# Performance work log

Hardware: AMD Instinct MI355X
Metric: run time of the kernel (lower is better)

The kernel has to match this reference:

```python
import jax, jax.numpy as jnp
import numpy as np

N_NODES = 100000
N_GRAPHS = 256
N_EDGES = 800000


def gcn_conv(x, W, b, src, dst):
    """PyG GCNConv: self-loops + symmetric deg^-1/2 normalization + scatter-add."""
    h = x @ W  # [N, F_out]
    # degree on graph with self-loops (edge weight 1)
    deg = jax.ops.segment_sum(jnp.ones((src.shape[0],), h.dtype), dst,
                              num_segments=N_NODES) + 1.0
    dinv = jax.lax.rsqrt(deg)  # deg^-1/2, deg >= 1 so finite
    norm = dinv[src] * dinv[dst]  # [E]
    msg = h[src] * norm[:, None]  # gather + scale, [E, F_out]
    agg = jax.ops.segment_sum(msg, dst, num_segments=N_NODES)
    # self-loop contribution: dinv[i]^2 * h[i]
    agg = agg + h * (dinv * dinv)[:, None]
    return agg + b


def setup_inputs() -> dict:
    key = jax.random.key(0)
    ks = jax.random.split(key, 16)
    inp = {
        "x": jax.random.normal(ks[0], (N_NODES, 114), jnp.float32),
        "edge_index": jax.random.randint(ks[1], (2, N_EDGES), 0, N_NODES, jnp.int64)
        if jax.config.jax_enable_x64 else jax.random.randint(ks[1], (2, N_EDGES), 0, N_NODES, jnp.int32),
        "batch": jnp.sort(jax.random.randint(ks[2], (N_NODES,), 0, N_GRAPHS,
                                             jnp.int32)),
        "W1": jax.random.normal(ks[3], (114, 230), jnp.float32) * 0.09,
        "b1": jax.random.normal(ks[4], (230,), jnp.float32) * 0.01,
        "W2": jax.random.normal(ks[5], (230, 115), jnp.float32) * 0.07,
        "b2": jax.random.normal(ks[6], (115,), jnp.float32) * 0.01,
        "Wg": jax.random.normal(ks[7], (115, 64), jnp.float32) * 0.09,
        "bg": jax.random.normal(ks[8], (64,), jnp.float32) * 0.01,
        "Wf": jax.random.normal(ks[9], (64, 32), jnp.float32) * 0.12,
        "bf": jax.random.normal(ks[10], (32,), jnp.float32) * 0.01,
        "Wo": jax.random.normal(ks[11], (32, 1), jnp.float32) * 0.17,
        "bo": jax.random.normal(ks[12], (1,), jnp.float32) * 0.01,
    }
    return inp


def reference(x, edge_index, batch, W1, b1, W2, b2, Wg, bg, Wf, bf, Wo, bo):
    src, dst = edge_index[0], edge_index[1]
    h = jax.nn.relu(gcn_conv(x, W1, b1, src, dst))
    # dropout p=0.2 is identity at inference (training=False)
    h = jax.nn.relu(gcn_conv(h, W2, b2, src, dst))
    # global max pool over graphs; h >= 0 after relu so clamp empty segments to 0
    pooled = jax.ops.segment_max(h, batch, num_segments=N_GRAPHS)
    pooled = jnp.maximum(pooled, 0.0)  # [G, 115]
    g = jax.nn.relu(pooled @ Wg + bg)
    g = jax.nn.relu(g @ Wf + bf)
    return g @ Wo + bo  # [G, 1]
```

## Files before the change

kernel.cpp:

```cpp
#include <hip/hip_runtime.h>
#include <hip/hip_bf16.h>
#include <hip/hip_fp16.h>

#define NN 100000
#define NG 256
#define NE 800000

constexpr int F0 = 114;
constexpr int F1 = 230;
constexpr int F2 = 115;
constexpr int MPAD = 100096;

typedef _Float16 __attribute__((ext_vector_type(8))) f16x8;
typedef __attribute__((ext_vector_type(4))) float f32x4;
typedef __attribute__((ext_vector_type(8))) unsigned short u16x8;

__device__ __forceinline__ unsigned short f2h_bits(float x) {
  _Float16 h = (_Float16)x;
  return __builtin_bit_cast(unsigned short, h);
}
__device__ __forceinline__ float h_bits2f(unsigned short u) {
  return (float)__builtin_bit_cast(_Float16, u);
}


__global__ void k_count(const int* __restrict__ dst, int* __restrict__ cnt) {
  int e = blockIdx.x * blockDim.x + threadIdx.x;
  if (e < NE) atomicAdd(&cnt[dst[e]], 1);
}

__global__ void k_dinv(const int* __restrict__ cnt, float* __restrict__ dinv) {
  int i = blockIdx.x * blockDim.x + threadIdx.x;
  if (i < NN) dinv[i] = rsqrtf((float)cnt[i] + 1.0f);
}

constexpr int SCAN_T = 256;
constexpr int SCAN_E = 1024;
constexpr int NB = (NN + SCAN_E - 1) / SCAN_E;

__global__ void k_scan1(const int* __restrict__ cnt, int* __restrict__ off,
                        int* __restrict__ bsum) {
  __shared__ int s[SCAN_T];
  int b = blockIdx.x, t = threadIdx.x;
  int base = b * SCAN_E + t * 4;
  int v0 = 0, v1 = 0, v2 = 0, v3 = 0;
  if (base + 0 < NN) v0 = cnt[base + 0];
  if (base + 1 < NN) v1 = cnt[base + 1];
  if (base + 2 < NN) v2 = cnt[base + 2];
  if (base + 3 < NN) v3 = cnt[base + 3];
  int sum = v0 + v1 + v2 + v3;
  s[t] = sum;
  __syncthreads();
  for (int ofs = 1; ofs < SCAN_T; ofs <<= 1) {
    int x = (t >= ofs) ? s[t - ofs] : 0;
    __syncthreads();
    s[t] += x;
    __syncthreads();
  }
  int excl = s[t] - sum;
  if (base + 0 < NN) off[base + 0] = excl;
  if (base + 1 < NN) off[base + 1] = excl + v0;
  if (base + 2 < NN) off[base + 2] = excl + v0 + v1;
  if (base + 3 < NN) off[base + 3] = excl + v0 + v1 + v2;
  if (t == SCAN_T - 1) bsum[b] = s[t];
}

__global__ void k_scan2(int* bsum) {
  __shared__ int ws[2];
  int t = threadIdx.x;
  int v = (t < NB) ? bsum[t] : 0;
  int orig = v;
  for (int o = 1; o < 64; o <<= 1) {
    int x = __shfl_up(v, o, 64);
    if ((t & 63) >= o) v += x;
  }
  if ((t & 63) == 63) ws[t >> 6] = v;
  __syncthreads();
  if (t >= 64) v += ws[0];
  if (t < NB) bsum[t] = v - orig;
}

__global__ void k_scan3(int* __restrict__ off, const int* __restrict__ bsum,
                        int* __restrict__ cur) {
  int i = blockIdx.x * blockDim.x + threadIdx.x;
  if (i < NN) {
    int v = off[i] + bsum[i / SCAN_E];
    off[i] = v;
    cur[i] = v;
  }
  if (i == NN) off[NN] = NE;
}

__global__ void k_place(const int* __restrict__ src, const int* __restrict__ dst,
                        int* __restrict__ cur, int* __restrict__ srcs) {
  int e = blockIdx.x * blockDim.x + threadIdx.x;
  if (e >= NE) return;
  int p = atomicAdd(&cur[dst[e]], 1);
  srcs[p] = src[e];
}


__global__ void k_prepx(const float* __restrict__ x, const float* __restrict__ dinv,
                        unsigned short* __restrict__ xd) {
  int n = blockIdx.x, f = threadIdx.x;
  float v = (f < F0) ? x[(size_t)n * F0 + f] * dinv[n] : 0.0f;
  xd[(size_t)n * 128 + f] = f2h_bits(v);
}


template <bool POOL>
__global__ __launch_bounds__(256) void k_gatherw(
    const unsigned short* __restrict__ tab, const float* __restrict__ dinv,
    const int* __restrict__ off, const int* __restrict__ srcs,
    const float* __restrict__ b2, const int* __restrict__ batch,
    unsigned short* __restrict__ outh, float* __restrict__ pooled) {
  __shared__ float smax[4][128];
  __shared__ int sg[4];
  int w = threadIdx.x >> 6, lane = threadIdx.x & 63;
  int n = blockIdx.x * 4 + w;
  int grp = lane >> 4, sub = lane & 15;
  int fb = sub * 8;

  float acc[8] = {0.f, 0.f, 0.f, 0.f, 0.f, 0.f, 0.f, 0.f};
  int j0 = off[n], j1 = off[n + 1];
  for (int base = j0; base <= j1; base += 16) {
    int row[4];
    u16x8 v[4];
    bool has[4];
#pragma unroll
    for (int c = 0; c < 4; ++c) {
      int je = base + c * 4 + grp;
      row[c] = (je < j1) ? srcs[je] : ((je == j1) ? n : -1);
      has[c] = row[c] >= 0;
    }
#pragma unroll
    for (int c = 0; c < 4; ++c)
      if (has[c]) v[c] = *(const u16x8*)&tab[(size_t)row[c] * 128 + fb];
#pragma unroll
    for (int c = 0; c < 4; ++c)
      if (has[c]) {
#pragma unroll
        for (int u = 0; u < 8; ++u) acc[u] += h_bits2f(v[c][u]);
      }
  }
#pragma unroll
  for (int u = 0; u < 8; ++u) {
    acc[u] += __shfl_xor(acc[u], 16);
    acc[u] += __shfl_xor(acc[u], 32);
  }
  float dn = dinv[n];

  if constexpr (!POOL) {
    if (grp == 0) {
      u16x8 o;
#pragma unroll
      for (int u = 0; u < 8; ++u) o[u] = f2h_bits(acc[u] * dn);
      *(u16x8*)&outh[(size_t)n * 128 + fb] = o;
    }
  } else {
    if (grp == 0) {
#pragma unroll
      for (int u = 0; u < 8; ++u) {
        int f = fb + u;
        float bb = (f < F2) ? b2[f] : 0.0f;
        smax[w][f] = fmaxf(acc[u] * dn + bb, 0.0f);
      }
      if (sub == 0) sg[w] = batch[n];
    }
    __syncthreads();
    int t = threadIdx.x;
    if (t < 128) {
      int g0 = sg[0];
      bool same = (sg[1] == g0) & (sg[2] == g0) & (sg[3] == g0);
      if (same) {
        float m = fmaxf(fmaxf(smax[0][t], smax[1][t]),
                        fmaxf(smax[2][t], smax[3][t]));
        if (t < F2 && m > 0.0f)
          atomicMax((int*)&pooled[g0 * F2 + t], __float_as_int(m));
      } else {
        for (int ww = 0; ww < 4; ++ww) {
          float m = smax[ww][t];
          if (t < F2 && m > 0.0f)
            atomicMax((int*)&pooled[sg[ww] * F2 + t], __float_as_int(m));
        }
      }
    }
  }
}


__global__ void k_prepB(const float* __restrict__ W, unsigned short* __restrict__ Bh,
                        unsigned short* __restrict__ Bl, int K, int N, int KP) {
  int n = blockIdx.x, k = threadIdx.x;
  float v = (k < K && n < N) ? W[(size_t)k * N + n] : 0.0f;
  unsigned short h = f2h_bits(v);
  unsigned short l = f2h_bits(v - h_bits2f(h));
  Bh[(size_t)n * KP + k] = h;
  Bl[(size_t)n * KP + k] = l;
}


__global__ __launch_bounds__(256, 3) void k_fused(
    const unsigned short* __restrict__ A,
    const unsigned short* __restrict__ B1h, const unsigned short* __restrict__ B1l,
    const unsigned short* __restrict__ B2h, const unsigned short* __restrict__ B2l,
    const float* __restrict__ b1, const float* __restrict__ dscale,
    unsigned short* __restrict__ td) {
  __shared__ char lds[49152];
  char* h1B = lds;
  char* Bs0 = lds + 16384;
  char* Bs1 = lds + 32768;

  const int t = threadIdx.x;
  const int m0 = blockIdx.x * 64;
  const int lane = t & 63, w = t >> 6;
  const int r = lane & 15;
  const int kq = lane >> 4;
  const int kb2 = kq * 16;
  const int kbu = kq * 8;
  const int rq = kq * 4;
  const int wc = w * 32;
  const int brow = t >> 1, bseg = t & 1;
  const int rb = brow * 128, swb = (brow & 7) << 4;

  const unsigned short* Ath = A + (size_t)(m0 + r) * 128 + kbu;

  f32x4 acc2[4][2];
#pragma unroll
  for (int i = 0; i < 4; ++i)
#pragma unroll
    for (int j = 0; j < 2; ++j) acc2[i][j] = (f32x4){0.f, 0.f, 0.f, 0.f};

  for (int h = 0; h < 2; ++h) {
    f32x4 acc[4][2];
#pragma unroll
    for (int i = 0; i < 4; ++i)
#pragma unroll
      for (int j = 0; j < 2; ++j) acc[i][j] = (f32x4){0.f, 0.f, 0.f, 0.f};

    for (int kc = 0; kc < 2; ++kc) {
      __syncthreads();
      {
        size_t gb = (size_t)(h * 128 + brow) * 128 + kc * 64 + bseg * 32;
#pragma unroll
        for (int v = 0; v < 4; ++v) {
          const int bo = rb + ((bseg * 64 + v * 16) ^ swb);
          *(u16x8*)(Bs0 + bo) = *(const u16x8*)&B1h[gb + v * 8];
          *(u16x8*)(Bs1 + bo) = *(const u16x8*)&B1l[gb + v * 8];
        }
      }
      __syncthreads();
#pragma unroll
      for (int ks = 0; ks < 2; ++ks) {
        f16x8 av[4], bh[2], bl[2];
#pragma unroll
        for (int i = 0; i < 4; ++i)
          av[i] = *(const f16x8*)&Ath[i * 2048 + kc * 64 + ks * 32];
#pragma unroll
        for (int j = 0; j < 2; ++j) {
          const int row = wc + j * 16 + r;
          const int bo = (ks * 64 + kb2) ^ ((row & 7) << 4);
          bh[j] = *(const f16x8*)(Bs0 + row * 128 + bo);
          bl[j] = *(const f16x8*)(Bs1 + row * 128 + bo);
        }
#pragma unroll
        for (int i = 0; i < 4; ++i)
#pragma unroll
          for (int j = 0; j < 2; ++j)
            acc[i][j] = __builtin_amdgcn_mfma_f32_16x16x32_f16(av[i], bl[j], acc[i][j], 0, 0, 0);
#pragma unroll
        for (int i = 0; i < 4; ++i)
#pragma unroll
          for (int j = 0; j < 2; ++j)
            acc[i][j] = __builtin_amdgcn_mfma_f32_16x16x32_f16(av[i], bh[j], acc[i][j], 0, 0, 0);
      }
    }

#pragma unroll
    for (int i = 0; i < 4; ++i)
#pragma unroll
      for (int j = 0; j < 2; ++j) {
        const int nl = wc + j * 16 + r;
        const int n = h * 128 + nl;
        const bool val = n < F1;
        const float bb = val ? b1[n] : 0.0f;
#pragma unroll
        for (int q = 0; q < 4; ++q) {
          const int ml = i * 16 + rq + q;
          const float v = val ? fmaxf(acc[i][j][q] + bb, 0.0f) : 0.0f;
          *(unsigned short*)(h1B + ml * 256 + ((nl * 2) ^ ((ml & 7) << 4))) = f2h_bits(v);
        }
      }

    for (int kc = 0; kc < 2; ++kc) {
      __syncthreads();
      {
        size_t gb = (size_t)brow * 256 + h * 128 + kc * 64 + bseg * 32;
#pragma unroll
        for (int v = 0; v < 4; ++v) {
          const int bo = rb + ((bseg * 64 + v * 16) ^ swb);
          *(u16x8*)(Bs0 + bo) = *(const u16x8*)&B2h[gb + v * 8];
          *(u16x8*)(Bs1 + bo) = *(const u16x8*)&B2l[gb + v * 8];
        }
      }
      __syncthreads();
#pragma unroll
      for (int ks = 0; ks < 2; ++ks) {
        f16x8 ah[4], bh[2], bl[2];
#pragma unroll
        for (int i = 0; i < 4; ++i) {
          const int row = i * 16 + r;
          ah[i] = *(const f16x8*)(h1B + row * 256 +
                                  ((kc * 128 + ks * 64 + kb2) ^ ((row & 7) << 4)));
        }
#pragma unroll
        for (int j = 0; j < 2; ++j) {
          const int row = wc + j * 16 + r;
          const int bo = (ks * 64 + kb2) ^ ((row & 7) << 4);
          bh[j] = *(const f16x8*)(Bs0 + row * 128 + bo);
          bl[j] = *(const f16x8*)(Bs1 + row * 128 + bo);
        }
#pragma unroll
        for (int i = 0; i < 4; ++i)
#pragma unroll
          for (int j = 0; j < 2; ++j)
            acc2[i][j] = __builtin_amdgcn_mfma_f32_16x16x32_f16(ah[i], bl[j], acc2[i][j], 0, 0, 0);
#pragma unroll
        for (int i = 0; i < 4; ++i)
#pragma unroll
          for (int j = 0; j < 2; ++j)
            acc2[i][j] = __builtin_amdgcn_mfma_f32_16x16x32_f16(ah[i], bh[j], acc2[i][j], 0, 0, 0);
      }
    }
  }

  __syncthreads();
#pragma unroll
  for (int i = 0; i < 4; ++i)
#pragma unroll
    for (int j = 0; j < 2; ++j) {
      const int nl = wc + j * 16 + r;
#pragma unroll
      for (int q = 0; q < 4; ++q) {
        const int ml = i * 16 + rq + q;
        const float v = acc2[i][j][q] * dscale[m0 + ml];
        *(unsigned short*)(h1B + ml * 256 + ((nl * 2) ^ ((ml & 7) << 4))) = f2h_bits(v);
      }
    }
  __syncthreads();
  {
    const int row = t >> 2, seg = t & 3;
    const int swz = (row & 7) << 4;
    const size_t dst = (size_t)(m0 + row) * 128 + seg * 32;
#pragma unroll
    for (int v = 0; v < 4; ++v) {
      u16x8 d = *(const u16x8*)(h1B + row * 256 + ((seg * 64 + v * 16) ^ swz));
      *(u16x8*)&td[dst + v * 8] = d;
    }
  }
}


__global__ void k_mlp(const float* __restrict__ pooled,
                      const float* __restrict__ Wg, const float* __restrict__ bg,
                      const float* __restrict__ Wf, const float* __restrict__ bf,
                      const float* __restrict__ Wo, const float* __restrict__ bo,
                      float* __restrict__ out) {
  __shared__ float sp[F2];
  __shared__ float sg[64];
  __shared__ float sf[32];
  int g = blockIdx.x, t = threadIdx.x;
  for (int f = t; f < F2; f += 64) sp[f] = pooled[g * F2 + f];
  __syncthreads();
  float a = bg[t];
  for (int k = 0; k < F2; ++k) a += sp[k] * Wg[k * 64 + t];
  sg[t] = fmaxf(a, 0.0f);
  __syncthreads();
  if (t < 32) {
    float c = bf[t];
    for (int k = 0; k < 64; ++k) c += sg[k] * Wf[k * 32 + t];
    sf[t] = fmaxf(c, 0.0f);
  }
  __syncthreads();
  if (t == 0) {
    float c = bo[0];
    for (int k = 0; k < 32; ++k) c += sf[k] * Wo[k];
    out[g] = c;
  }
}


extern "C" void kernel_launch(void* const* d_in, const int* in_sizes, int n_in,
                              void* d_out, int out_size, void* d_ws, size_t ws_size,
                              hipStream_t stream) {
  const float* x  = (const float*)d_in[0];
  const int* ei   = (const int*)d_in[1];
  const int* batch = (const int*)d_in[2];
  const float* W1 = (const float*)d_in[3];
  const float* b1 = (const float*)d_in[4];
  const float* W2 = (const float*)d_in[5];
  const float* b2 = (const float*)d_in[6];
  const float* Wg = (const float*)d_in[7];
  const float* bg = (const float*)d_in[8];
  const float* Wf = (const float*)d_in[9];
  const float* bf = (const float*)d_in[10];
  const float* Wo = (const float*)d_in[11];
  const float* bo = (const float*)d_in[12];
  const int* src = ei;
  const int* dst = ei + NE;

  char* p = (char*)d_ws;
  auto alloc4 = [&](size_t units) { void* r = p; p += units * 4; return r; };
  float* dinv  = (float*)alloc4(100224);
  int* cnt     = (int*)alloc4(100224);
  int* off     = (int*)alloc4(100352);
  int* cur     = (int*)alloc4(100224);
  int* bsum    = (int*)alloc4(128);
  int* srcs    = (int*)alloc4(NE);
  unsigned short* xd   = (unsigned short*)alloc4((size_t)NN * 128 / 2);
  unsigned short* aggX = (unsigned short*)alloc4((size_t)MPAD * 128 / 2);
  unsigned short* td   = (unsigned short*)alloc4((size_t)MPAD * 128 / 2);
  unsigned short* Bt1h = (unsigned short*)alloc4(256 * 128 / 2);
  unsigned short* Bt1l = (unsigned short*)alloc4(256 * 128 / 2);
  unsigned short* Bt2h = (unsigned short*)alloc4(128 * 256 / 2);
  unsigned short* Bt2l = (unsigned short*)alloc4(128 * 256 / 2);
  float* pooled = (float*)alloc4((size_t)NG * F2);

  hipMemsetAsync(cnt, 0, 100224 * sizeof(int), stream);
  hipMemsetAsync(pooled, 0, (size_t)NG * F2 * sizeof(float), stream);

  k_count<<<(NE + 255) / 256, 256, 0, stream>>>(dst, cnt);
  k_dinv<<<(NN + 255) / 256, 256, 0, stream>>>(cnt, dinv);
  k_scan1<<<NB, SCAN_T, 0, stream>>>(cnt, off, bsum);
  k_scan2<<<1, 128, 0, stream>>>(bsum);
  k_scan3<<<(NN + 256) / 256, 256, 0, stream>>>(off, bsum, cur);
  k_place<<<(NE + 255) / 256, 256, 0, stream>>>(src, dst, cur, srcs);

  k_prepB<<<256, 128, 0, stream>>>(W1, Bt1h, Bt1l, F0, F1, 128);
  k_prepB<<<128, 256, 0, stream>>>(W2, Bt2h, Bt2l, F1, F2, 256);

  k_prepx<<<NN, 128, 0, stream>>>(x, dinv, xd);
  k_gatherw<false><<<NN / 4, 256, 0, stream>>>(xd, dinv, off, srcs,
                                               nullptr, nullptr, aggX, nullptr);

  k_fused<<<MPAD / 64, 256, 0, stream>>>(aggX, Bt1h, Bt1l, Bt2h, Bt2l,
                                         b1, dinv, td);

  k_gatherw<true><<<NN / 4, 256, 0, stream>>>(td, dinv, off, srcs,
                                              b2, batch, nullptr, pooled);

  k_mlp<<<NG, 64, 0, stream>>>(pooled, Wg, bg, Wf, bf, Wo, bo, (float*)d_out);
}
```

Measured before the change: 337.2 us.

## Merge small setup kernels and restructure fused GEMM to stage A and full h1 in LDS

Folds the dinv computation into the first scan kernel and merges the two weight-prep kernels into one launch, which removes kernel launches. In the fused two-layer GEMM, the A tile is now staged through LDS with a swizzle instead of being read directly from global memory per wave. The whole 256-wide hidden tile is kept in LDS so the second GEMM runs once over K=256 after both halves of the first, rather than being interleaved per half. LDS use grows from 48KB to 72KB and the launch-bounds occupancy hint is dropped, which may lower occupancy.

```diff
diff --git a/kernel.cpp b/kernel.cpp
--- a/kernel.cpp
+++ b/kernel.cpp
@@ -29,17 +29,12 @@
   if (e < NE) atomicAdd(&cnt[dst[e]], 1);
 }
 
-__global__ void k_dinv(const int* __restrict__ cnt, float* __restrict__ dinv) {
-  int i = blockIdx.x * blockDim.x + threadIdx.x;
-  if (i < NN) dinv[i] = rsqrtf((float)cnt[i] + 1.0f);
-}
-
 constexpr int SCAN_T = 256;
 constexpr int SCAN_E = 1024;
 constexpr int NB = (NN + SCAN_E - 1) / SCAN_E;
 
 __global__ void k_scan1(const int* __restrict__ cnt, int* __restrict__ off,
-                        int* __restrict__ bsum) {
+                        int* __restrict__ bsum, float* __restrict__ dinv) {
   __shared__ int s[SCAN_T];
   int b = blockIdx.x, t = threadIdx.x;
   int base = b * SCAN_E + t * 4;
@@ -48,6 +43,10 @@
   if (base + 1 < NN) v1 = cnt[base + 1];
   if (base + 2 < NN) v2 = cnt[base + 2];
   if (base + 3 < NN) v3 = cnt[base + 3];
+  if (base + 0 < NN) dinv[base + 0] = rsqrtf((float)v0 + 1.0f);
+  if (base + 1 < NN) dinv[base + 1] = rsqrtf((float)v1 + 1.0f);
+  if (base + 2 < NN) dinv[base + 2] = rsqrtf((float)v2 + 1.0f);
+  if (base + 3 < NN) dinv[base + 3] = rsqrtf((float)v3 + 1.0f);
   int sum = v0 + v1 + v2 + v3;
   s[t] = sum;
   __syncthreads();
@@ -189,41 +188,51 @@
 }
 
 
-__global__ void k_prepB(const float* __restrict__ W, unsigned short* __restrict__ Bh,
-                        unsigned short* __restrict__ Bl, int K, int N, int KP) {
-  int n = blockIdx.x, k = threadIdx.x;
-  float v = (k < K && n < N) ? W[(size_t)k * N + n] : 0.0f;
-  unsigned short h = f2h_bits(v);
-  unsigned short l = f2h_bits(v - h_bits2f(h));
-  Bh[(size_t)n * KP + k] = h;
-  Bl[(size_t)n * KP + k] = l;
-}
-
-
-__global__ __launch_bounds__(256, 3) void k_fused(
+__global__ void k_prepB2(const float* __restrict__ W1, const float* __restrict__ W2,
+                         unsigned short* __restrict__ B1h, unsigned short* __restrict__ B1l,
+                         unsigned short* __restrict__ B2h, unsigned short* __restrict__ B2l) {
+  int b = blockIdx.x, t = threadIdx.x;
+  if (b < 128) {
+    int n = b * 2 + (t >> 7), k = t & 127;
+    float v = (k < F0 && n < F1) ? W1[(size_t)k * F1 + n] : 0.0f;
+    unsigned short h = f2h_bits(v);
+    unsigned short l = f2h_bits(v - h_bits2f(h));
+    B1h[(size_t)n * 128 + k] = h;
+    B1l[(size_t)n * 128 + k] = l;
+  } else {
+    int n = b - 128, k = t;
+    float v = (k < F1 && n < F2) ? W2[(size_t)k * F2 + n] : 0.0f;
+    unsigned short h = f2h_bits(v);
+    unsigned short l = f2h_bits(v - h_bits2f(h));
+    B2h[(size_t)n * 256 + k] = h;
+    B2l[(size_t)n * 256 + k] = l;
+  }
+}
+
+
+__global__ __launch_bounds__(256) void k_fused(
     const unsigned short* __restrict__ A,
     const unsigned short* __restrict__ B1h, const unsigned short* __restrict__ B1l,
     const unsigned short* __restrict__ B2h, const unsigned short* __restrict__ B2l,
     const float* __restrict__ b1, const float* __restrict__ dscale,
     unsigned short* __restrict__ td) {
-  __shared__ char lds[49152];
+  __shared__ char lds[73728];
   char* h1B = lds;
-  char* Bs0 = lds + 16384;
-  char* Bs1 = lds + 32768;
+  char* AsB = lds + 32768;
+  char* Bs0 = lds + 40960;
+  char* Bs1 = lds + 57344;
 
   const int t = threadIdx.x;
   const int m0 = blockIdx.x * 64;
   const int lane = t & 63, w = t >> 6;
   const int r = lane & 15;
   const int kq = lane >> 4;
-  const int kb2 = kq * 16;
-  const int kbu = kq * 8;
+  const int kb16 = kq * 16;
   const int rq = kq * 4;
   const int wc = w * 32;
-  const int brow = t >> 1, bseg = t & 1;
-  const int rb = brow * 128, swb = (brow & 7) << 4;
-
-  const unsigned short* Ath = A + (size_t)(m0 + r) * 128 + kbu;
+  const int swr = (r & 7) << 4;
+  const int arow = t >> 2, aq = t & 3, aswz = (arow & 7) << 4;
+  const int brow = t >> 1, bseg = t & 1, bswz = (brow & 7) << 4;
 
   f32x4 acc2[4][2];
 #pragma unroll
@@ -241,12 +250,15 @@
     for (int kc = 0; kc < 2; ++kc) {
       __syncthreads();
       {
+        size_t ga = (size_t)(m0 + arow) * 128 + kc * 64 + aq * 16;
+        *(u16x8*)(AsB + arow * 128 + ((aq * 32) ^ aswz))      = *(const u16x8*)&A[ga];
+        *(u16x8*)(AsB + arow * 128 + ((aq * 32 + 16) ^ aswz)) = *(const u16x8*)&A[ga + 8];
         size_t gb = (size_t)(h * 128 + brow) * 128 + kc * 64 + bseg * 32;
 #pragma unroll
         for (int v = 0; v < 4; ++v) {
-          const int bo = rb + ((bseg * 64 + v * 16) ^ swb);
-          *(u16x8*)(Bs0 + bo) = *(const u16x8*)&B1h[gb + v * 8];
-          *(u16x8*)(Bs1 + bo) = *(const u16x8*)&B1l[gb + v * 8];
+          const int bo = (bseg * 64 + v * 16) ^ bswz;
+          *(u16x8*)(Bs0 + brow * 128 + bo) = *(const u16x8*)&B1h[gb + v * 8];
+          *(u16x8*)(Bs1 + brow * 128 + bo) = *(const u16x8*)&B1l[gb + v * 8];
         }
       }
       __syncthreads();
@@ -255,11 +267,11 @@
         f16x8 av[4], bh[2], bl[2];
 #pragma unroll
         for (int i = 0; i < 4; ++i)
-          av[i] = *(const f16x8*)&Ath[i * 2048 + kc * 64 + ks * 32];
+          av[i] = *(const f16x8*)(AsB + (i * 16 + r) * 128 + ((ks * 64 + kb16) ^ swr));
 #pragma unroll
         for (int j = 0; j < 2; ++j) {
           const int row = wc + j * 16 + r;
-          const int bo = (ks * 64 + kb2) ^ ((row & 7) << 4);
+          const int bo = (ks * 64 + kb16) ^ swr;
           bh[j] = *(const f16x8*)(Bs0 + row * 128 + bo);
           bl[j] = *(const f16x8*)(Bs1 + row * 128 + bo);
         }
@@ -288,49 +300,48 @@
         for (int q = 0; q < 4; ++q) {
           const int ml = i * 16 + rq + q;
           const float v = val ? fmaxf(acc[i][j][q] + bb, 0.0f) : 0.0f;
-          *(unsigned short*)(h1B + ml * 256 + ((nl * 2) ^ ((ml & 7) << 4))) = f2h_bits(v);
+          *(unsigned short*)(h1B + ml * 512 + ((n * 2) ^ ((ml & 7) << 4))) = f2h_bits(v);
         }
       }
-
-    for (int kc = 0; kc < 2; ++kc) {
-      __syncthreads();
-      {
-        size_t gb = (size_t)brow * 256 + h * 128 + kc * 64 + bseg * 32;
-#pragma unroll
-        for (int v = 0; v < 4; ++v) {
-          const int bo = rb + ((bseg * 64 + v * 16) ^ swb);
-          *(u16x8*)(Bs0 + bo) = *(const u16x8*)&B2h[gb + v * 8];
-          *(u16x8*)(Bs1 + bo) = *(const u16x8*)&B2l[gb + v * 8];
-        }
-      }
-      __syncthreads();
-#pragma unroll
-      for (int ks = 0; ks < 2; ++ks) {
-        f16x8 ah[4], bh[2], bl[2];
-#pragma unroll
-        for (int i = 0; i < 4; ++i) {
-          const int row = i * 16 + r;
-          ah[i] = *(const f16x8*)(h1B + row * 256 +
-                                  ((kc * 128 + ks * 64 + kb2) ^ ((row & 7) << 4)));
-        }
-#pragma unroll
-        for (int j = 0; j < 2; ++j) {
-          const int row = wc + j * 16 + r;
-          const int bo = (ks * 64 + kb2) ^ ((row & 7) << 4);
-          bh[j] = *(const f16x8*)(Bs0 + row * 128 + bo);
-          bl[j] = *(const f16x8*)(Bs1 + row * 128 + bo);
-        }
-#pragma unroll
-        for (int i = 0; i < 4; ++i)
-#pragma unroll
-          for (int j = 0; j < 2; ++j)
-            acc2[i][j] = __builtin_amdgcn_mfma_f32_16x16x32_f16(ah[i], bl[j], acc2[i][j], 0, 0, 0);
-#pragma unroll
-        for (int i = 0; i < 4; ++i)
-#pragma unroll
-          for (int j = 0; j < 2; ++j)
-            acc2[i][j] = __builtin_amdgcn_mfma_f32_16x16x32_f16(ah[i], bh[j], acc2[i][j], 0, 0, 0);
-      }
+  }
+
+  for (int kc = 0; kc < 4; ++kc) {
+    __syncthreads();
+    {
+      size_t gb = (size_t)brow * 256 + kc * 64 + bseg * 32;
+#pragma unroll
+      for (int v = 0; v < 4; ++v) {
+        const int bo = (bseg * 64 + v * 16) ^ bswz;
+        *(u16x8*)(Bs0 + brow * 128 + bo) = *(const u16x8*)&B2h[gb + v * 8];
+        *(u16x8*)(Bs1 + brow * 128 + bo) = *(const u16x8*)&B2l[gb + v * 8];
+      }
+    }
+    __syncthreads();
+#pragma unroll
+    for (int ks = 0; ks < 2; ++ks) {
+      f16x8 ah[4], bh[2], bl[2];
+#pragma unroll
+      for (int i = 0; i < 4; ++i) {
+        const int row = i * 16 + r;
+        ah[i] = *(const f16x8*)(h1B + row * 512 + ((kc * 128 + ks * 64 + kb16) ^ swr));
+      }
+#pragma unroll
+      for (int j = 0; j < 2; ++j) {
+        const int row = wc + j * 16 + r;
+        const int bo = (ks * 64 + kb16) ^ swr;
+        bh[j] = *(const f16x8*)(Bs0 + row * 128 + bo);
+        bl[j] = *(const f16x8*)(Bs1 + row * 128 + bo);
+      }
+#pragma unroll
+      for (int i = 0; i < 4; ++i)
+#pragma unroll
+        for (int j = 0; j < 2; ++j)
+          acc2[i][j] = __builtin_amdgcn_mfma_f32_16x16x32_f16(ah[i], bl[j], acc2[i][j], 0, 0, 0);
+#pragma unroll
+      for (int i = 0; i < 4; ++i)
+#pragma unroll
+        for (int j = 0; j < 2; ++j)
+          acc2[i][j] = __builtin_amdgcn_mfma_f32_16x16x32_f16(ah[i], bh[j], acc2[i][j], 0, 0, 0);
     }
   }
 
@@ -344,7 +355,7 @@
       for (int q = 0; q < 4; ++q) {
         const int ml = i * 16 + rq + q;
         const float v = acc2[i][j][q] * dscale[m0 + ml];
-        *(unsigned short*)(h1B + ml * 256 + ((nl * 2) ^ ((ml & 7) << 4))) = f2h_bits(v);
+        *(unsigned short*)(h1B + ml * 512 + ((nl * 2) ^ ((ml & 7) << 4))) = f2h_bits(v);
       }
     }
   __syncthreads();
@@ -354,7 +365,7 @@
     const size_t dst = (size_t)(m0 + row) * 128 + seg * 32;
 #pragma unroll
     for (int v = 0; v < 4; ++v) {
-      u16x8 d = *(const u16x8*)(h1B + row * 256 + ((seg * 64 + v * 16) ^ swz));
+      u16x8 d = *(const u16x8*)(h1B + row * 512 + ((seg * 64 + v * 16) ^ swz));
       *(u16x8*)&td[dst + v * 8] = d;
     }
   }
@@ -430,14 +441,12 @@
   hipMemsetAsync(pooled, 0, (size_t)NG * F2 * sizeof(float), stream);
 
   k_count<<<(NE + 255) / 256, 256, 0, stream>>>(dst, cnt);
-  k_dinv<<<(NN + 255) / 256, 256, 0, stream>>>(cnt, dinv);
-  k_scan1<<<NB, SCAN_T, 0, stream>>>(cnt, off, bsum);
+  k_scan1<<<NB, SCAN_T, 0, stream>>>(cnt, off, bsum, dinv);
   k_scan2<<<1, 128, 0, stream>>>(bsum);
   k_scan3<<<(NN + 256) / 256, 256, 0, stream>>>(off, bsum, cur);
   k_place<<<(NE + 255) / 256, 256, 0, stream>>>(src, dst, cur, srcs);
 
-  k_prepB<<<256, 128, 0, stream>>>(W1, Bt1h, Bt1l, F0, F1, 128);
-  k_prepB<<<128, 256, 0, stream>>>(W2, Bt2h, Bt2l, F1, F2, 256);
+  k_prepB2<<<256, 256, 0, stream>>>(W1, W2, Bt1h, Bt1l, Bt2h, Bt2l);
 
   k_prepx<<<NN, 128, 0, stream>>>(x, dinv, xd);
   k_gatherw<false><<<NN / 4, 256, 0, stream>>>(xd, dinv, off, srcs,
```

Measured after the change: 304.1 us. -9.8%, faster.
